# Optimization experiments

Hardware: AMD Instinct MI355X
Metric: run time of the kernel (lower is better)

## Reference

```python
import jax, jax.numpy as jnp
import numpy as np

N = 20000        # nodes
NHID = 128       # hidden channels per head
HEADS = 4
E = 320000       # edges (before self-loops)
NLAYERS = 4
NCLASS = 40
DT, ALPHA, GAMMA = 1.0, 1.0, 1.0
NEG_SLOPE = 0.2  # PyG GATConv default


def setup_inputs() -> dict:
    key = jax.random.key(0)
    ks = jax.random.split(key, 8)
    s = 1.0 / np.sqrt(NHID)
    x = jax.random.normal(ks[0], (N, NHID), jnp.float32)
    src = jax.random.randint(ks[1], (E,), 0, N, dtype=jnp.int32)
    dst = jax.random.randint(ks[2], (E,), 0, N, dtype=jnp.int32)
    W = jax.random.normal(ks[3], (NHID, HEADS * NHID), jnp.float32) * s
    att_src = jax.random.normal(ks[4], (HEADS, NHID), jnp.float32) * s
    att_dst = jax.random.normal(ks[5], (HEADS, NHID), jnp.float32) * s
    bias = jnp.zeros((HEADS * NHID,), jnp.float32)
    Wr = jax.random.normal(ks[6], (NCLASS, NHID), jnp.float32) * s
    br = jnp.zeros((NCLASS,), jnp.float32)
    return {"x": x, "src": src, "dst": dst, "W": W, "att_src": att_src,
            "att_dst": att_dst, "bias": bias, "Wr": Wr, "br": br}


def reference(x, src, dst, W, att_src, att_dst, bias, Wr, br):
    # add self loops (PyG GATConv default)
    loop = jnp.arange(N, dtype=src.dtype)
    s_idx = jnp.concatenate([src, loop])
    d_idx = jnp.concatenate([dst, loop])

    def gat(X):
        # X: [N, NHID] -> out: [N, HEADS*NHID] (head-major, as PyG concat)
        h = (X @ W).reshape(N, HEADS, NHID)                  # [N,H,C]
        a_s = jnp.einsum('nhc,hc->nh', h, att_src)            # [N,H]
        a_d = jnp.einsum('nhc,hc->nh', h, att_dst)            # [N,H]
        e = jax.nn.leaky_relu(a_s[s_idx] + a_d[d_idx], NEG_SLOPE)  # [Etot,H]
        m = jax.ops.segment_max(e, d_idx, num_segments=N)     # scatter-softmax
        ex = jnp.exp(e - m[d_idx])
        den = jax.ops.segment_sum(ex, d_idx, num_segments=N)
        alpha = ex / den[d_idx]                               # [Etot,H]
        msg = h[s_idx] * alpha[..., None]                     # [Etot,H,C]
        out = jax.ops.segment_sum(msg, d_idx, num_segments=N)  # [N,H,C]
        return out.reshape(N, HEADS * NHID) + bias

    def step(carry, _):
        X, Y = carry
        # view(N, -1, nheads).mean(-1) on head-major [N, H*C] layout
        agg = jax.nn.elu(gat(X)).reshape(N, NHID, HEADS).mean(axis=-1)
        Y2 = Y + DT * (agg - ALPHA * Y - GAMMA * X)
        X2 = X + DT * Y2
        return (X2, Y2), (X2, Y2)

    (Xf, Yf), (Xs, Ys) = jax.lax.scan(step, (x, x), None, length=NLAYERS)
    X_all = jnp.concatenate([x[:, None], jnp.moveaxis(Xs, 0, 1)], axis=1)  # [N,L+1,C]
    Y_all = jnp.concatenate([x[:, None], jnp.moveaxis(Ys, 0, 1)], axis=1)
    out = Xf @ Wr.T + br                                     # [N, NCLASS]
    return out, X_all, Y_all
```

## Files before the change

### kernel.cpp

```cpp
#include <hip/hip_runtime.h>

typedef unsigned short u16;
typedef unsigned int u32;

#define N_NODES 20000
#define NE 320000
#define NLAYERS 4
#define NCLASS 40
#define NEG_SLOPE 0.2f
#define LSTRIDE ((NLAYERS + 1) * 128)

typedef __bf16 bf16x8 __attribute__((ext_vector_type(8)));
typedef float f32x4 __attribute__((ext_vector_type(4)));

__device__ inline u16 f2bf(float f) {
    u32 u = __float_as_uint(f);
    return (u16)((u + 0x7fffu + ((u >> 16) & 1u)) >> 16);
}
__device__ inline float bf2f(u16 u) { return __uint_as_float(((u32)u) << 16); }

__global__ void k_init(const float* __restrict__ x, u16* __restrict__ Xbf,
                       float* __restrict__ Xall, float* __restrict__ Yall,
                       int* __restrict__ counts) {
    int t = blockIdx.x * 256 + threadIdx.x;
    if (t >= N_NODES * 128) return;
    if (t < N_NODES) counts[t] = 1;
    float v = x[t];
    Xbf[t] = f2bf(v);
    int n = t >> 7, c = t & 127;
    int ob = n * LSTRIDE + c;
    Xall[ob] = v;
    Yall[ob] = v;
}

__global__ void k_trans(const float* __restrict__ W, u16* __restrict__ Wt) {
    int t = blockIdx.x * 256 + threadIdx.x;
    int k = t >> 9, col = t & 511;
    Wt[col * 128 + k] = f2bf(W[t]);
}

__global__ __launch_bounds__(256) void k_fold(const float* __restrict__ W,
                                              const float* __restrict__ att_s,
                                              const float* __restrict__ att_d,
                                              float* __restrict__ Vs, float* __restrict__ Vd) {
    int wid = (blockIdx.x * 256 + threadIdx.x) >> 6;
    int lane = threadIdx.x & 63;
    int t = wid >> 2, hd = wid & 3;
    float w0 = W[t * 512 + hd * 128 + lane];
    float w1 = W[t * 512 + hd * 128 + 64 + lane];
    float s1 = w0 * att_s[hd * 128 + lane] + w1 * att_s[hd * 128 + 64 + lane];
    float s2 = w0 * att_d[hd * 128 + lane] + w1 * att_d[hd * 128 + 64 + lane];
    for (int off = 32; off; off >>= 1) {
        s1 += __shfl_xor(s1, off);
        s2 += __shfl_xor(s2, off);
    }
    if (lane == 0) {
        Vs[t * 4 + hd] = s1;
        Vd[t * 4 + hd] = s2;
    }
}

__global__ void k_count(const int* __restrict__ dst, int* __restrict__ counts) {
    int t = blockIdx.x * 256 + threadIdx.x;
    if (t < NE) atomicAdd(&counts[dst[t]], 1);
}
__global__ void k_scan(const int* __restrict__ counts, int* __restrict__ indptr,
                       int* __restrict__ cursor) {
    __shared__ int part[1024];
    int t = threadIdx.x;
    const int CH = 20;
    int c0 = t * CH;
    int s = 0;
    for (int i = 0; i < CH; i++) {
        int idx = c0 + i;
        if (idx < N_NODES) s += counts[idx];
    }
    part[t] = s;
    __syncthreads();
    for (int off = 1; off < 1024; off <<= 1) {
        int v = 0;
        if (t >= off) v = part[t - off];
        __syncthreads();
        if (t >= off) part[t] += v;
        __syncthreads();
    }
    int ex = (t == 0) ? 0 : part[t - 1];
    for (int i = 0; i < CH; i++) {
        int idx = c0 + i;
        if (idx < N_NODES) {
            indptr[idx] = ex;
            cursor[idx] = ex;
            ex += counts[idx];
        }
    }
    if (t == 1023) indptr[N_NODES] = part[1023];
}
__global__ void k_scatter(const int* __restrict__ src, const int* __restrict__ dst,
                          int* __restrict__ cursor, int* __restrict__ esrc) {
    int t = blockIdx.x * 256 + threadIdx.x;
    if (t >= NE + N_NODES) return;
    int s, d;
    if (t < NE) { s = src[t]; d = dst[t]; }
    else { s = d = t - NE; }
    int pos = atomicAdd(&cursor[d], 1);
    esrc[pos] = s;
}

__global__ __launch_bounds__(256) void k_att(const float* __restrict__ Xall, int layer,
                                             const float* __restrict__ Vs,
                                             const float* __restrict__ Vd,
                                             float* __restrict__ a_s, float* __restrict__ a_d) {
    int wid = (blockIdx.x * 256 + threadIdx.x) >> 6;
    int lane = threadIdx.x & 63;
    const float* Xr = Xall + wid * LSTRIDE + layer * 128;
    float x0 = Xr[lane], x1 = Xr[64 + lane];
    f32x4 vs0 = *(const f32x4*)(Vs + lane * 4), vs1 = *(const f32x4*)(Vs + (64 + lane) * 4);
    f32x4 vd0 = *(const f32x4*)(Vd + lane * 4), vd1 = *(const f32x4*)(Vd + (64 + lane) * 4);
    f32x4 ps = x0 * vs0 + x1 * vs1;
    f32x4 pd = x0 * vd0 + x1 * vd1;
    for (int off = 32; off; off >>= 1)
        for (int c = 0; c < 4; c++) {
            ps[c] += __shfl_xor(ps[c], off);
            pd[c] += __shfl_xor(pd[c], off);
        }
    if (lane == 0) {
        *(f32x4*)(a_s + wid * 4) = ps;
        *(f32x4*)(a_d + wid * 4) = pd;
    }
}

__global__ __launch_bounds__(256) void k_aggr(
    const int* __restrict__ indptr, const int* __restrict__ esrc,
    const float* __restrict__ a_s, const float* __restrict__ a_d,
    const u16* __restrict__ Xbf, u16* __restrict__ Xagg) {
    __shared__ int s_sh[4][66];
    __shared__ alignas(16) float al_sh[4][66][4];
    int d = (blockIdx.x * 256 + threadIdx.x) >> 6;
    int lane = threadIdx.x & 63;
    int w = threadIdx.x >> 6;
    int start = indptr[d], end = indptr[d + 1];
    int deg = end - start;
    f32x4 ad = *(const f32x4*)(a_d + d * 4);
    f32x4 accA = {0.f, 0.f, 0.f, 0.f};
    f32x4 accB = {0.f, 0.f, 0.f, 0.f};

    auto chunk_aggr = [&](int cnt) {
        int s_cur = s_sh[w][0];
        f32x4 al_cur = *(const f32x4*)&al_sh[w][0][0];
        u32 xv = *(const u32*)(Xbf + s_cur * 128 + lane * 2);
        for (int i = 0; i < cnt; i++) {
            int s_nxt = s_sh[w][i + 1];
            f32x4 al_nxt = *(const f32x4*)&al_sh[w][i + 1][0];
            u32 xv_n = *(const u32*)(Xbf + s_nxt * 128 + lane * 2);
            float x0 = __uint_as_float(xv << 16);
            float x1 = __uint_as_float(xv & 0xffff0000u);
            accA += al_cur * x0;
            accB += al_cur * x1;
            xv = xv_n;
            al_cur = al_nxt;
        }
    };

    if (deg <= 64) {
        int j = start + lane;
        int s = 0;
        f32x4 e = {-1e30f, -1e30f, -1e30f, -1e30f};
        if (j < end) {
            s = esrc[j];
            f32x4 as = *(const f32x4*)(a_s + s * 4);
            for (int c = 0; c < 4; c++) {
                float v = as[c] + ad[c];
                e[c] = v > 0.f ? v : NEG_SLOPE * v;
            }
        }
        f32x4 mx = e;
        for (int off = 32; off; off >>= 1)
            for (int c = 0; c < 4; c++) mx[c] = fmaxf(mx[c], __shfl_xor(mx[c], off));
        f32x4 p;
        for (int c = 0; c < 4; c++) p[c] = __expf(e[c] - mx[c]);
        f32x4 den = p;
        for (int off = 32; off; off >>= 1)
            for (int c = 0; c < 4; c++) den[c] += __shfl_xor(den[c], off);
        f32x4 alpha;
        for (int c = 0; c < 4; c++) alpha[c] = p[c] * (1.f / den[c]);
        s_sh[w][lane] = s;
        *(f32x4*)&al_sh[w][lane][0] = alpha;
        if (lane == 63) {
            s_sh[w][64] = 0;
            f32x4 z = {0.f, 0.f, 0.f, 0.f};
            *(f32x4*)&al_sh[w][64][0] = z;
        }
        __builtin_amdgcn_wave_barrier();
        chunk_aggr(deg);
    } else {
        f32x4 mx = {-1e30f, -1e30f, -1e30f, -1e30f};
        for (int j = start + lane; j < end; j += 64) {
            int s = esrc[j];
            f32x4 e = *(const f32x4*)(a_s + s * 4) + ad;
            for (int c = 0; c < 4; c++) {
                float v = e[c];
                v = v > 0.f ? v : NEG_SLOPE * v;
                mx[c] = fmaxf(mx[c], v);
            }
        }
        for (int off = 32; off; off >>= 1)
            for (int c = 0; c < 4; c++) mx[c] = fmaxf(mx[c], __shfl_xor(mx[c], off));
        f32x4 den = {0.f, 0.f, 0.f, 0.f};
        for (int j = start + lane; j < end; j += 64) {
            int s = esrc[j];
            f32x4 e = *(const f32x4*)(a_s + s * 4) + ad;
            for (int c = 0; c < 4; c++) {
                float v = e[c];
                v = v > 0.f ? v : NEG_SLOPE * v;
                den[c] += __expf(v - mx[c]);
            }
        }
        for (int off = 32; off; off >>= 1)
            for (int c = 0; c < 4; c++) den[c] += __shfl_xor(den[c], off);
        f32x4 rd;
        for (int c = 0; c < 4; c++) rd[c] = 1.f / den[c];
        for (int base = start; base < end; base += 64) {
            int cnt = min(64, end - base);
            int jj = base + lane;
            int s = 0;
            f32x4 alpha = {0.f, 0.f, 0.f, 0.f};
            if (jj < end) {
                s = esrc[jj];
                f32x4 e = *(const f32x4*)(a_s + s * 4) + ad;
                for (int c = 0; c < 4; c++) {
                    float v = e[c];
                    v = v > 0.f ? v : NEG_SLOPE * v;
                    alpha[c] = __expf(v - mx[c]) * rd[c];
                }
            }
            s_sh[w][lane] = s;
            *(f32x4*)&al_sh[w][lane][0] = alpha;
            if (lane == 63) {
                s_sh[w][64] = 0;
                f32x4 z = {0.f, 0.f, 0.f, 0.f};
                *(f32x4*)&al_sh[w][64][0] = z;
            }
            __builtin_amdgcn_wave_barrier();
            chunk_aggr(cnt);
            __builtin_amdgcn_wave_barrier();
        }
    }

    u16* xo = Xagg + d * 512 + lane * 2;
    for (int hh = 0; hh < 4; hh++) {
        u32 pk = (u32)f2bf(accA[hh]) | ((u32)f2bf(accB[hh]) << 16);
        *(u32*)(xo + hh * 128) = pk;
    }
}

__global__ __launch_bounds__(512) void k_fuse(
    const u16* __restrict__ Xagg, const u16* __restrict__ Wt,
    const float* __restrict__ bias,
    float* __restrict__ Xall, float* __restrict__ Yall, u16* __restrict__ Xbf,
    float* __restrict__ a_s_nxt, float* __restrict__ a_d_nxt,
    const float* __restrict__ Vs, const float* __restrict__ Vd,
    int layer, int do_logits) {
    __shared__ u16 As[16 * 520];
    __shared__ float G[16 * 528];
    __shared__ float aggbuf[16 * 130];
    const int t = threadIdx.x;
    const int r0 = blockIdx.x * 16;
    const int wv = t >> 6, lane = t & 63;
    const int h = wv >> 1, colhalf = wv & 1;
    const int lrow = lane & 15, quad = lane >> 4;

    bf16x8 bfr[16];
    {
        const u16* Wb = Wt + (h * 128 + colhalf * 64) * 128;
        for (int k4 = 0; k4 < 4; k4++)
            for (int ni = 0; ni < 4; ni++)
                bfr[k4 * 4 + ni] =
                    *(const bf16x8*)(Wb + (ni * 16 + lrow) * 128 + k4 * 32 + quad * 8);
    }
    for (int i = 0; i < 2; i++) {
        int flat = i * 512 + t;
        int row = flat >> 6, kc = flat & 63;
        *(uint4*)(As + row * 520 + kc * 8) = *(const uint4*)(Xagg + (r0 + row) * 512 + kc * 8);
    }
    __syncthreads();
    f32x4 acc[4] = {};
    for (int k4 = 0; k4 < 4; k4++) {
        bf16x8 a = *(const bf16x8*)(As + lrow * 520 + h * 128 + k4 * 32 + quad * 8);
        for (int ni = 0; ni < 4; ni++)
            acc[ni] = __builtin_amdgcn_mfma_f32_16x16x32_bf16(a, bfr[k4 * 4 + ni], acc[ni], 0, 0, 0);
    }
    for (int ni = 0; ni < 4; ni++) {
        int c = colhalf * 64 + ni * 16 + lrow;
        float bv = bias[h * 128 + c];
        for (int r = 0; r < 4; r++) {
            float v = acc[ni][r] + bv;
            v = v > 0.f ? v : __expf(v) - 1.f;
            G[(quad * 4 + r) * 528 + h * 128 + c] = v;
        }
    }
    __syncthreads();
    {
        int c = t & 127, rg = t >> 7;
        int hh = c >> 5, cc = (c & 31) * 4;
        for (int rr = 0; rr < 4; rr++) {
            int row = rg * 4 + rr;
            f32x4 gp = *(const f32x4*)&G[row * 528 + hh * 128 + cc];
            float agg = 0.25f * (gp[0] + gp[1] + gp[2] + gp[3]);
            aggbuf[row * 130 + c] = agg;
            int node = r0 + row;
            int xo = node * LSTRIDE + layer * 128 + c;
            int no = node * LSTRIDE + (layer + 1) * 128 + c;
            float xp = Xall[xo];
            Xall[no] = agg;
            Yall[no] = agg - xp;
            Xbf[node * 128 + c] = f2bf(agg);
        }
    }
    if (do_logits) {
        __syncthreads();
        f32x4 vs0 = *(const f32x4*)(Vs + lane * 4), vs1 = *(const f32x4*)(Vs + (64 + lane) * 4);
        f32x4 vd0 = *(const f32x4*)(Vd + lane * 4), vd1 = *(const f32x4*)(Vd + (64 + lane) * 4);
        for (int rr = 0; rr < 2; rr++) {
            int row = wv * 2 + rr;
            float x0 = aggbuf[row * 130 + lane], x1 = aggbuf[row * 130 + 64 + lane];
            f32x4 ps = x0 * vs0 + x1 * vs1;
            f32x4 pd = x0 * vd0 + x1 * vd1;
            for (int off = 32; off; off >>= 1)
                for (int c2 = 0; c2 < 4; c2++) {
                    ps[c2] += __shfl_xor(ps[c2], off);
                    pd[c2] += __shfl_xor(pd[c2], off);
                }
            if (lane == 0) {
                int node = r0 + row;
                *(f32x4*)(a_s_nxt + node * 4) = ps;
                *(f32x4*)(a_d_nxt + node * 4) = pd;
            }
        }
    }
}

__global__ __launch_bounds__(256) void k_out(const float* __restrict__ Xall,
                                             const float* __restrict__ Wr,
                                             const float* __restrict__ br,
                                             float* __restrict__ out) {
    __shared__ float Xs[4][128];
    int wave = threadIdx.x >> 6, lane = threadIdx.x & 63;
    int n = blockIdx.x * 4 + wave;
    const float* Xr = Xall + n * LSTRIDE + NLAYERS * 128;
    Xs[wave][lane] = Xr[lane];
    Xs[wave][64 + lane] = Xr[64 + lane];
    __syncthreads();
    if (lane < NCLASS) {
        float acc = 0.f;
        for (int kc = 0; kc < 32; kc++) {
            f32x4 wv = *(const f32x4*)(Wr + lane * 128 + kc * 4);
            for (int q = 0; q < 4; q++) acc += Xs[wave][kc * 4 + q] * wv[q];
        }
        out[n * NCLASS + lane] = acc + br[lane];
    }
}

extern "C" void kernel_launch(void* const* d_in, const int* in_sizes, int n_in,
                              void* d_out, int out_size, void* d_ws, size_t ws_size,
                              hipStream_t stream) {
    const float* x = (const float*)d_in[0];
    const int* src = (const int*)d_in[1];
    const int* dst = (const int*)d_in[2];
    const float* W = (const float*)d_in[3];
    const float* att_s = (const float*)d_in[4];
    const float* att_d = (const float*)d_in[5];
    const float* bias = (const float*)d_in[6];
    const float* Wr = (const float*)d_in[7];
    const float* br = (const float*)d_in[8];

    float* out = (float*)d_out;
    float* Xall = out + (size_t)N_NODES * NCLASS;
    float* Yall = Xall + (size_t)N_NODES * LSTRIDE;

    char* p = (char*)d_ws;
    auto alloc = [&](size_t bytes) -> char* {
        char* r = p;
        p += (bytes + 255) & ~(size_t)255;
        return r;
    };
    u16* Xbf = (u16*)alloc((size_t)N_NODES * 128 * 2);
    u16* Xagg = (u16*)alloc((size_t)N_NODES * 512 * 2);
    u16* Wt = (u16*)alloc(512 * 128 * 2);
    float* a_sA = (float*)alloc((size_t)N_NODES * 4 * 4);
    float* a_dA = (float*)alloc((size_t)N_NODES * 4 * 4);
    float* a_sB = (float*)alloc((size_t)N_NODES * 4 * 4);
    float* a_dB = (float*)alloc((size_t)N_NODES * 4 * 4);
    float* Vs = (float*)alloc(128 * 4 * 4);
    float* Vd = (float*)alloc(128 * 4 * 4);
    int* indptr = (int*)alloc((N_NODES + 1) * 4);
    int* cursor = (int*)alloc(N_NODES * 4);
    int* counts = (int*)alloc(N_NODES * 4);
    int* esrc = (int*)alloc((size_t)(NE + N_NODES) * 4);

    k_init<<<(N_NODES * 128 + 255) / 256, 256, 0, stream>>>(x, Xbf, Xall, Yall, counts);
    k_trans<<<(512 * 128) / 256, 256, 0, stream>>>(W, Wt);
    k_fold<<<128, 256, 0, stream>>>(W, att_s, att_d, Vs, Vd);
    k_count<<<(NE + 255) / 256, 256, 0, stream>>>(dst, counts);
    k_scan<<<1, 1024, 0, stream>>>(counts, indptr, cursor);
    k_scatter<<<(NE + N_NODES + 255) / 256, 256, 0, stream>>>(src, dst, cursor, esrc);

    k_att<<<N_NODES / 4, 256, 0, stream>>>(Xall, 0, Vs, Vd, a_sA, a_dA);

    for (int layer = 0; layer < NLAYERS; layer++) {
        const float* as_r = (layer & 1) ? a_sB : a_sA;
        const float* ad_r = (layer & 1) ? a_dB : a_dA;
        float* as_w = (layer & 1) ? a_sA : a_sB;
        float* ad_w = (layer & 1) ? a_dA : a_dB;
        k_aggr<<<N_NODES / 4, 256, 0, stream>>>(indptr, esrc, as_r, ad_r, Xbf, Xagg);
        k_fuse<<<N_NODES / 16, 512, 0, stream>>>(Xagg, Wt, bias, Xall, Yall, Xbf,
                                                 as_w, ad_w, Vs, Vd, layer,
                                                 (layer + 1 < NLAYERS) ? 1 : 0);
    }
    k_out<<<N_NODES / 4, 256, 0, stream>>>(Xall, Wr, br, out);
}
```

Before: 500.8 us.

## Fuse edge aggregation with MFMA projection per layer and merge setup kernels

Merges the per-layer aggregation and GEMM/ELU/update kernels into one kernel. Each wave aggregates two destination nodes and writes the bf16 aggregate straight to shared memory, so the Xagg global round trip goes away. The bf16 feature buffer is double-buffered so that other blocks never read rows that are already being overwritten. The setup kernels are grouped into two multi-role launches, with a memset and a +1 in the scan standing in for self-loop counts. The head-mean now uses shuffles in place of a large shared G buffer, and W fragments are read from global memory inside the MFMA loop instead of being preloaded into registers.

```diff
diff --git a/kernel.cpp b/kernel.cpp
--- a/kernel.cpp
+++ b/kernel.cpp
@@ -17,84 +17,110 @@
     u32 u = __float_as_uint(f);
     return (u16)((u + 0x7fffu + ((u >> 16) & 1u)) >> 16);
 }
-__device__ inline float bf2f(u16 u) { return __uint_as_float(((u32)u) << 16); }
-
-__global__ void k_init(const float* __restrict__ x, u16* __restrict__ Xbf,
-                       float* __restrict__ Xall, float* __restrict__ Yall,
-                       int* __restrict__ counts) {
-    int t = blockIdx.x * 256 + threadIdx.x;
-    if (t >= N_NODES * 128) return;
-    if (t < N_NODES) counts[t] = 1;
-    float v = x[t];
-    Xbf[t] = f2bf(v);
-    int n = t >> 7, c = t & 127;
-    int ob = n * LSTRIDE + c;
-    Xall[ob] = v;
-    Yall[ob] = v;
-}
-
-__global__ void k_trans(const float* __restrict__ W, u16* __restrict__ Wt) {
-    int t = blockIdx.x * 256 + threadIdx.x;
-    int k = t >> 9, col = t & 511;
-    Wt[col * 128 + k] = f2bf(W[t]);
-}
-
-__global__ __launch_bounds__(256) void k_fold(const float* __restrict__ W,
-                                              const float* __restrict__ att_s,
-                                              const float* __restrict__ att_d,
-                                              float* __restrict__ Vs, float* __restrict__ Vd) {
-    int wid = (blockIdx.x * 256 + threadIdx.x) >> 6;
-    int lane = threadIdx.x & 63;
-    int t = wid >> 2, hd = wid & 3;
-    float w0 = W[t * 512 + hd * 128 + lane];
-    float w1 = W[t * 512 + hd * 128 + 64 + lane];
-    float s1 = w0 * att_s[hd * 128 + lane] + w1 * att_s[hd * 128 + 64 + lane];
-    float s2 = w0 * att_d[hd * 128 + lane] + w1 * att_d[hd * 128 + 64 + lane];
-    for (int off = 32; off; off >>= 1) {
-        s1 += __shfl_xor(s1, off);
-        s2 += __shfl_xor(s2, off);
-    }
-    if (lane == 0) {
-        Vs[t * 4 + hd] = s1;
-        Vd[t * 4 + hd] = s2;
-    }
-}
-
-__global__ void k_count(const int* __restrict__ dst, int* __restrict__ counts) {
-    int t = blockIdx.x * 256 + threadIdx.x;
-    if (t < NE) atomicAdd(&counts[dst[t]], 1);
-}
-__global__ void k_scan(const int* __restrict__ counts, int* __restrict__ indptr,
-                       int* __restrict__ cursor) {
-    __shared__ int part[1024];
-    int t = threadIdx.x;
-    const int CH = 20;
-    int c0 = t * CH;
-    int s = 0;
-    for (int i = 0; i < CH; i++) {
-        int idx = c0 + i;
-        if (idx < N_NODES) s += counts[idx];
-    }
-    part[t] = s;
-    __syncthreads();
-    for (int off = 1; off < 1024; off <<= 1) {
-        int v = 0;
-        if (t >= off) v = part[t - off];
+__device__ inline u32 pack2bf(float lo, float hi) {
+    return (u32)f2bf(lo) | ((u32)f2bf(hi) << 16);
+}
+
+#define P1_INIT 10000
+#define P1_TRANS 256
+#define P1_FOLD 128
+#define P1_COUNT 1250
+__global__ __launch_bounds__(256) void k_pre1(
+    const float* __restrict__ x, const int* __restrict__ dst,
+    const float* __restrict__ W, const float* __restrict__ att_s,
+    const float* __restrict__ att_d,
+    u16* __restrict__ Xbf, float* __restrict__ Xall, float* __restrict__ Yall,
+    u16* __restrict__ Wt, float* __restrict__ Vs, float* __restrict__ Vd,
+    int* __restrict__ counts) {
+    int b = blockIdx.x;
+    if (b < P1_INIT) {
+        int t = b * 256 + threadIdx.x;
+        float v = x[t];
+        Xbf[t] = f2bf(v);
+        int n = t >> 7, c = t & 127;
+        int ob = n * LSTRIDE + c;
+        Xall[ob] = v;
+        Yall[ob] = v;
+    } else if (b < P1_INIT + P1_TRANS) {
+        int t = (b - P1_INIT) * 256 + threadIdx.x;
+        int k = t >> 9, col = t & 511;
+        Wt[col * 128 + k] = f2bf(W[t]);
+    } else if (b < P1_INIT + P1_TRANS + P1_FOLD) {
+        int wid = ((b - P1_INIT - P1_TRANS) * 256 + threadIdx.x) >> 6;
+        int lane = threadIdx.x & 63;
+        int t = wid >> 2, hd = wid & 3;
+        float w0 = W[t * 512 + hd * 128 + lane];
+        float w1 = W[t * 512 + hd * 128 + 64 + lane];
+        float s1 = w0 * att_s[hd * 128 + lane] + w1 * att_s[hd * 128 + 64 + lane];
+        float s2 = w0 * att_d[hd * 128 + lane] + w1 * att_d[hd * 128 + 64 + lane];
+        for (int off = 32; off; off >>= 1) {
+            s1 += __shfl_xor(s1, off);
+            s2 += __shfl_xor(s2, off);
+        }
+        if (lane == 0) {
+            Vs[t * 4 + hd] = s1;
+            Vd[t * 4 + hd] = s2;
+        }
+    } else {
+        int t = (b - P1_INIT - P1_TRANS - P1_FOLD) * 256 + threadIdx.x;
+        atomicAdd(&counts[dst[t]], 1);
+    }
+}
+
+__global__ __launch_bounds__(1024) void k_pre2(
+    const int* __restrict__ counts, int* __restrict__ indptr, int* __restrict__ cursor,
+    const float* __restrict__ x, const float* __restrict__ Vs, const float* __restrict__ Vd,
+    float* __restrict__ a_s, float* __restrict__ a_d) {
+    if (blockIdx.x == 0) {
+        __shared__ int part[1024];
+        int t = threadIdx.x;
+        const int CH = 20;
+        int c0 = t * CH;
+        int s = 0;
+        for (int i = 0; i < CH; i++) {
+            int idx = c0 + i;
+            if (idx < N_NODES) s += counts[idx] + 1;
+        }
+        part[t] = s;
         __syncthreads();
-        if (t >= off) part[t] += v;
-        __syncthreads();
-    }
-    int ex = (t == 0) ? 0 : part[t - 1];
-    for (int i = 0; i < CH; i++) {
-        int idx = c0 + i;
-        if (idx < N_NODES) {
-            indptr[idx] = ex;
-            cursor[idx] = ex;
-            ex += counts[idx];
-        }
-    }
-    if (t == 1023) indptr[N_NODES] = part[1023];
-}
+        for (int off = 1; off < 1024; off <<= 1) {
+            int v = 0;
+            if (t >= off) v = part[t - off];
+            __syncthreads();
+            if (t >= off) part[t] += v;
+            __syncthreads();
+        }
+        int ex = (t == 0) ? 0 : part[t - 1];
+        for (int i = 0; i < CH; i++) {
+            int idx = c0 + i;
+            if (idx < N_NODES) {
+                indptr[idx] = ex;
+                cursor[idx] = ex;
+                ex += counts[idx] + 1;
+            }
+        }
+        if (t == 1023) indptr[N_NODES] = part[1023];
+    } else {
+        int wave = threadIdx.x >> 6, lane = threadIdx.x & 63;
+        int n = (blockIdx.x - 1) * 16 + wave;
+        const float* Xr = x + n * 128;
+        float x0 = Xr[lane], x1 = Xr[64 + lane];
+        f32x4 vs0 = *(const f32x4*)(Vs + lane * 4), vs1 = *(const f32x4*)(Vs + (64 + lane) * 4);
+        f32x4 vd0 = *(const f32x4*)(Vd + lane * 4), vd1 = *(const f32x4*)(Vd + (64 + lane) * 4);
+        f32x4 ps = x0 * vs0 + x1 * vs1;
+        f32x4 pd = x0 * vd0 + x1 * vd1;
+        for (int off = 32; off; off >>= 1)
+            for (int c = 0; c < 4; c++) {
+                ps[c] += __shfl_xor(ps[c], off);
+                pd[c] += __shfl_xor(pd[c], off);
+            }
+        if (lane == 0) {
+            *(f32x4*)(a_s + n * 4) = ps;
+            *(f32x4*)(a_d + n * 4) = pd;
+        }
+    }
+}
+
 __global__ void k_scatter(const int* __restrict__ src, const int* __restrict__ dst,
                           int* __restrict__ cursor, int* __restrict__ esrc) {
     int t = blockIdx.x * 256 + threadIdx.x;
@@ -106,66 +132,37 @@
     esrc[pos] = s;
 }
 
-__global__ __launch_bounds__(256) void k_att(const float* __restrict__ Xall, int layer,
-                                             const float* __restrict__ Vs,
-                                             const float* __restrict__ Vd,
-                                             float* __restrict__ a_s, float* __restrict__ a_d) {
-    int wid = (blockIdx.x * 256 + threadIdx.x) >> 6;
-    int lane = threadIdx.x & 63;
-    const float* Xr = Xall + wid * LSTRIDE + layer * 128;
-    float x0 = Xr[lane], x1 = Xr[64 + lane];
-    f32x4 vs0 = *(const f32x4*)(Vs + lane * 4), vs1 = *(const f32x4*)(Vs + (64 + lane) * 4);
-    f32x4 vd0 = *(const f32x4*)(Vd + lane * 4), vd1 = *(const f32x4*)(Vd + (64 + lane) * 4);
-    f32x4 ps = x0 * vs0 + x1 * vs1;
-    f32x4 pd = x0 * vd0 + x1 * vd1;
-    for (int off = 32; off; off >>= 1)
-        for (int c = 0; c < 4; c++) {
-            ps[c] += __shfl_xor(ps[c], off);
-            pd[c] += __shfl_xor(pd[c], off);
-        }
-    if (lane == 0) {
-        *(f32x4*)(a_s + wid * 4) = ps;
-        *(f32x4*)(a_d + wid * 4) = pd;
-    }
-}
-
-__global__ __launch_bounds__(256) void k_aggr(
+__global__ __launch_bounds__(512) void k_layer(
     const int* __restrict__ indptr, const int* __restrict__ esrc,
     const float* __restrict__ a_s, const float* __restrict__ a_d,
-    const u16* __restrict__ Xbf, u16* __restrict__ Xagg) {
-    __shared__ int s_sh[4][66];
-    __shared__ alignas(16) float al_sh[4][66][4];
-    int d = (blockIdx.x * 256 + threadIdx.x) >> 6;
-    int lane = threadIdx.x & 63;
-    int w = threadIdx.x >> 6;
-    int start = indptr[d], end = indptr[d + 1];
-    int deg = end - start;
-    f32x4 ad = *(const f32x4*)(a_d + d * 4);
-    f32x4 accA = {0.f, 0.f, 0.f, 0.f};
-    f32x4 accB = {0.f, 0.f, 0.f, 0.f};
-
-    auto chunk_aggr = [&](int cnt) {
-        int s_cur = s_sh[w][0];
-        f32x4 al_cur = *(const f32x4*)&al_sh[w][0][0];
-        u32 xv = *(const u32*)(Xbf + s_cur * 128 + lane * 2);
-        for (int i = 0; i < cnt; i++) {
-            int s_nxt = s_sh[w][i + 1];
-            f32x4 al_nxt = *(const f32x4*)&al_sh[w][i + 1][0];
-            u32 xv_n = *(const u32*)(Xbf + s_nxt * 128 + lane * 2);
-            float x0 = __uint_as_float(xv << 16);
-            float x1 = __uint_as_float(xv & 0xffff0000u);
-            accA += al_cur * x0;
-            accB += al_cur * x1;
-            xv = xv_n;
-            al_cur = al_nxt;
-        }
-    };
-
-    if (deg <= 64) {
-        int j = start + lane;
+    const u16* __restrict__ XbfR, const u16* __restrict__ Wt,
+    const float* __restrict__ bias,
+    float* __restrict__ Xall, float* __restrict__ Yall, u16* __restrict__ XbfW,
+    float* __restrict__ a_s_nxt, float* __restrict__ a_d_nxt,
+    const float* __restrict__ Vs, const float* __restrict__ Vd,
+    int layer, int do_logits) {
+    __shared__ int s_sh[8][2][66];
+    __shared__ alignas(16) float al_sh[8][2][66][4];
+    __shared__ u16 As[16 * 520];
+    __shared__ float aggbuf[16 * 130];
+    const int t = threadIdx.x;
+    const int r0 = blockIdx.x * 16;
+    const int w = t >> 6, lane = t & 63;
+
+    f32x4 acc00 = {0.f, 0.f, 0.f, 0.f}, acc01 = {0.f, 0.f, 0.f, 0.f};
+    f32x4 acc10 = {0.f, 0.f, 0.f, 0.f}, acc11 = {0.f, 0.f, 0.f, 0.f};
+    int d0 = r0 + w * 2;
+    int st0 = indptr[d0], en0 = indptr[d0 + 1], en1 = indptr[d0 + 2];
+    int st1 = en0;
+    int deg0 = en0 - st0, deg1 = en1 - st1;
+    f32x4 ad0 = *(const f32x4*)(a_d + d0 * 4);
+    f32x4 ad1 = *(const f32x4*)(a_d + d0 * 4 + 4);
+
+    auto prep = [&](int nd, int st, int en, f32x4 ad) {
+        int j = st + lane;
         int s = 0;
         f32x4 e = {-1e30f, -1e30f, -1e30f, -1e30f};
-        if (j < end) {
+        if (j < en) {
             s = esrc[j];
             f32x4 as = *(const f32x4*)(a_s + s * 4);
             for (int c = 0; c < 4; c++) {
@@ -183,18 +180,31 @@
             for (int c = 0; c < 4; c++) den[c] += __shfl_xor(den[c], off);
         f32x4 alpha;
         for (int c = 0; c < 4; c++) alpha[c] = p[c] * (1.f / den[c]);
-        s_sh[w][lane] = s;
-        *(f32x4*)&al_sh[w][lane][0] = alpha;
+        s_sh[w][nd][lane] = s;
+        *(f32x4*)al_sh[w][nd][lane] = alpha;
         if (lane == 63) {
-            s_sh[w][64] = 0;
+            s_sh[w][nd][64] = 0;
             f32x4 z = {0.f, 0.f, 0.f, 0.f};
-            *(f32x4*)&al_sh[w][64][0] = z;
-        }
-        __builtin_amdgcn_wave_barrier();
-        chunk_aggr(deg);
-    } else {
+            *(f32x4*)al_sh[w][nd][64] = z;
+        }
+    };
+    auto chunk1 = [&](int nd, int cnt, f32x4& aL, f32x4& aH) {
+        int sc = s_sh[w][nd][0];
+        f32x4 al = *(const f32x4*)al_sh[w][nd][0];
+        u32 xv = *(const u32*)(XbfR + sc * 128 + lane * 2);
+        for (int i = 0; i < cnt; i++) {
+            int sn = s_sh[w][nd][i + 1];
+            f32x4 an = *(const f32x4*)al_sh[w][nd][i + 1];
+            u32 xn = *(const u32*)(XbfR + sn * 128 + lane * 2);
+            aL += al * __uint_as_float(xv << 16);
+            aH += al * __uint_as_float(xv & 0xffff0000u);
+            xv = xn;
+            al = an;
+        }
+    };
+    auto gen = [&](int nd, int st, int en, f32x4 ad, f32x4& aL, f32x4& aH) {
         f32x4 mx = {-1e30f, -1e30f, -1e30f, -1e30f};
-        for (int j = start + lane; j < end; j += 64) {
+        for (int j = st + lane; j < en; j += 64) {
             int s = esrc[j];
             f32x4 e = *(const f32x4*)(a_s + s * 4) + ad;
             for (int c = 0; c < 4; c++) {
@@ -206,7 +216,7 @@
         for (int off = 32; off; off >>= 1)
             for (int c = 0; c < 4; c++) mx[c] = fmaxf(mx[c], __shfl_xor(mx[c], off));
         f32x4 den = {0.f, 0.f, 0.f, 0.f};
-        for (int j = start + lane; j < end; j += 64) {
+        for (int j = st + lane; j < en; j += 64) {
             int s = esrc[j];
             f32x4 e = *(const f32x4*)(a_s + s * 4) + ad;
             for (int c = 0; c < 4; c++) {
@@ -219,12 +229,12 @@
             for (int c = 0; c < 4; c++) den[c] += __shfl_xor(den[c], off);
         f32x4 rd;
         for (int c = 0; c < 4; c++) rd[c] = 1.f / den[c];
-        for (int base = start; base < end; base += 64) {
-            int cnt = min(64, end - base);
+        for (int base = st; base < en; base += 64) {
+            int cnt = min(64, en - base);
             int jj = base + lane;
             int s = 0;
             f32x4 alpha = {0.f, 0.f, 0.f, 0.f};
-            if (jj < end) {
+            if (jj < en) {
                 s = esrc[jj];
                 f32x4 e = *(const f32x4*)(a_s + s * 4) + ad;
                 for (int c = 0; c < 4; c++) {
@@ -233,95 +243,101 @@
                     alpha[c] = __expf(v - mx[c]) * rd[c];
                 }
             }
-            s_sh[w][lane] = s;
-            *(f32x4*)&al_sh[w][lane][0] = alpha;
+            s_sh[w][nd][lane] = s;
+            *(f32x4*)al_sh[w][nd][lane] = alpha;
             if (lane == 63) {
-                s_sh[w][64] = 0;
+                s_sh[w][nd][64] = 0;
                 f32x4 z = {0.f, 0.f, 0.f, 0.f};
-                *(f32x4*)&al_sh[w][64][0] = z;
+                *(f32x4*)al_sh[w][nd][64] = z;
             }
             __builtin_amdgcn_wave_barrier();
-            chunk_aggr(cnt);
+            chunk1(nd, cnt, aL, aH);
             __builtin_amdgcn_wave_barrier();
         }
-    }
-
-    u16* xo = Xagg + d * 512 + lane * 2;
-    for (int hh = 0; hh < 4; hh++) {
-        u32 pk = (u32)f2bf(accA[hh]) | ((u32)f2bf(accB[hh]) << 16);
-        *(u32*)(xo + hh * 128) = pk;
-    }
-}
-
-__global__ __launch_bounds__(512) void k_fuse(
-    const u16* __restrict__ Xagg, const u16* __restrict__ Wt,
-    const float* __restrict__ bias,
-    float* __restrict__ Xall, float* __restrict__ Yall, u16* __restrict__ Xbf,
-    float* __restrict__ a_s_nxt, float* __restrict__ a_d_nxt,
-    const float* __restrict__ Vs, const float* __restrict__ Vd,
-    int layer, int do_logits) {
-    __shared__ u16 As[16 * 520];
-    __shared__ float G[16 * 528];
-    __shared__ float aggbuf[16 * 130];
-    const int t = threadIdx.x;
-    const int r0 = blockIdx.x * 16;
-    const int wv = t >> 6, lane = t & 63;
-    const int h = wv >> 1, colhalf = wv & 1;
+    };
+
+    if (deg0 <= 64 && deg1 <= 64) {
+        prep(0, st0, en0, ad0);
+        prep(1, st1, en1, ad1);
+        __builtin_amdgcn_wave_barrier();
+        int cm = deg0 > deg1 ? deg0 : deg1;
+        int sA = s_sh[w][0][0], sB = s_sh[w][1][0];
+        f32x4 aA = *(const f32x4*)al_sh[w][0][0];
+        f32x4 aB = *(const f32x4*)al_sh[w][1][0];
+        u32 xA = *(const u32*)(XbfR + sA * 128 + lane * 2);
+        u32 xB = *(const u32*)(XbfR + sB * 128 + lane * 2);
+        for (int i = 0; i < cm; i++) {
+            int sA2 = s_sh[w][0][i + 1], sB2 = s_sh[w][1][i + 1];
+            f32x4 aA2 = *(const f32x4*)al_sh[w][0][i + 1];
+            f32x4 aB2 = *(const f32x4*)al_sh[w][1][i + 1];
+            u32 xA2 = *(const u32*)(XbfR + sA2 * 128 + lane * 2);
+            u32 xB2 = *(const u32*)(XbfR + sB2 * 128 + lane * 2);
+            acc00 += aA * __uint_as_float(xA << 16);
+            acc01 += aA * __uint_as_float(xA & 0xffff0000u);
+            acc10 += aB * __uint_as_float(xB << 16);
+            acc11 += aB * __uint_as_float(xB & 0xffff0000u);
+            xA = xA2; aA = aA2; xB = xB2; aB = aB2;
+        }
+    } else {
+        gen(0, st0, en0, ad0, acc00, acc01);
+        gen(1, st1, en1, ad1, acc10, acc11);
+    }
+
+    {
+        u16* a0 = As + (w * 2) * 520 + lane * 2;
+        u16* a1 = As + (w * 2 + 1) * 520 + lane * 2;
+        for (int h = 0; h < 4; h++) {
+            *(u32*)(a0 + h * 128) = pack2bf(acc00[h], acc01[h]);
+            *(u32*)(a1 + h * 128) = pack2bf(acc10[h], acc11[h]);
+        }
+    }
+    __syncthreads();
+
+    const int h = w >> 1, colhalf = w & 1;
     const int lrow = lane & 15, quad = lane >> 4;
-
-    bf16x8 bfr[16];
-    {
-        const u16* Wb = Wt + (h * 128 + colhalf * 64) * 128;
-        for (int k4 = 0; k4 < 4; k4++)
-            for (int ni = 0; ni < 4; ni++)
-                bfr[k4 * 4 + ni] =
-                    *(const bf16x8*)(Wb + (ni * 16 + lrow) * 128 + k4 * 32 + quad * 8);
-    }
-    for (int i = 0; i < 2; i++) {
-        int flat = i * 512 + t;
-        int row = flat >> 6, kc = flat & 63;
-        *(uint4*)(As + row * 520 + kc * 8) = *(const uint4*)(Xagg + (r0 + row) * 512 + kc * 8);
-    }
-    __syncthreads();
-    f32x4 acc[4] = {};
+    f32x4 macc[4] = {};
     for (int k4 = 0; k4 < 4; k4++) {
         bf16x8 a = *(const bf16x8*)(As + lrow * 520 + h * 128 + k4 * 32 + quad * 8);
-        for (int ni = 0; ni < 4; ni++)
-            acc[ni] = __builtin_amdgcn_mfma_f32_16x16x32_bf16(a, bfr[k4 * 4 + ni], acc[ni], 0, 0, 0);
+        for (int ni = 0; ni < 4; ni++) {
+            bf16x8 bfrag = *(const bf16x8*)(Wt + (h * 128 + colhalf * 64 + ni * 16 + lrow) * 128 +
+                                            k4 * 32 + quad * 8);
+            macc[ni] = __builtin_amdgcn_mfma_f32_16x16x32_bf16(a, bfrag, macc[ni], 0, 0, 0);
+        }
     }
     for (int ni = 0; ni < 4; ni++) {
-        int c = colhalf * 64 + ni * 16 + lrow;
-        float bv = bias[h * 128 + c];
+        float bv = bias[h * 128 + colhalf * 64 + ni * 16 + lrow];
         for (int r = 0; r < 4; r++) {
-            float v = acc[ni][r] + bv;
+            float v = macc[ni][r] + bv;
             v = v > 0.f ? v : __expf(v) - 1.f;
-            G[(quad * 4 + r) * 528 + h * 128 + c] = v;
+            v += __shfl_xor(v, 1);
+            v += __shfl_xor(v, 2);
+            if ((lrow & 3) == 0) {
+                int row = quad * 4 + r;
+                int cO = h * 32 + colhalf * 16 + ni * 4 + (lrow >> 2);
+                aggbuf[row * 130 + cO] = 0.25f * v;
+            }
         }
     }
     __syncthreads();
+
     {
         int c = t & 127, rg = t >> 7;
-        int hh = c >> 5, cc = (c & 31) * 4;
         for (int rr = 0; rr < 4; rr++) {
             int row = rg * 4 + rr;
-            f32x4 gp = *(const f32x4*)&G[row * 528 + hh * 128 + cc];
-            float agg = 0.25f * (gp[0] + gp[1] + gp[2] + gp[3]);
-            aggbuf[row * 130 + c] = agg;
+            float agg = aggbuf[row * 130 + c];
             int node = r0 + row;
             int xo = node * LSTRIDE + layer * 128 + c;
-            int no = node * LSTRIDE + (layer + 1) * 128 + c;
             float xp = Xall[xo];
-            Xall[no] = agg;
-            Yall[no] = agg - xp;
-            Xbf[node * 128 + c] = f2bf(agg);
+            Xall[xo + 128] = agg;
+            Yall[xo + 128] = agg - xp;
+            XbfW[node * 128 + c] = f2bf(agg);
         }
     }
     if (do_logits) {
-        __syncthreads();
         f32x4 vs0 = *(const f32x4*)(Vs + lane * 4), vs1 = *(const f32x4*)(Vs + (64 + lane) * 4);
         f32x4 vd0 = *(const f32x4*)(Vd + lane * 4), vd1 = *(const f32x4*)(Vd + (64 + lane) * 4);
         for (int rr = 0; rr < 2; rr++) {
-            int row = wv * 2 + rr;
+            int row = w * 2 + rr;
             float x0 = aggbuf[row * 130 + lane], x1 = aggbuf[row * 130 + 64 + lane];
             f32x4 ps = x0 * vs0 + x1 * vs1;
             f32x4 pd = x0 * vd0 + x1 * vd1;
@@ -383,8 +399,8 @@
         p += (bytes + 255) & ~(size_t)255;
         return r;
     };
-    u16* Xbf = (u16*)alloc((size_t)N_NODES * 128 * 2);
-    u16* Xagg = (u16*)alloc((size_t)N_NODES * 512 * 2);
+    u16* XbfA = (u16*)alloc((size_t)N_NODES * 128 * 2);
+    u16* XbfB = (u16*)alloc((size_t)N_NODES * 128 * 2);
     u16* Wt = (u16*)alloc(512 * 128 * 2);
     float* a_sA = (float*)alloc((size_t)N_NODES * 4 * 4);
     float* a_dA = (float*)alloc((size_t)N_NODES * 4 * 4);
@@ -397,24 +413,22 @@
     int* counts = (int*)alloc(N_NODES * 4);
     int* esrc = (int*)alloc((size_t)(NE + N_NODES) * 4);
 
-    k_init<<<(N_NODES * 128 + 255) / 256, 256, 0, stream>>>(x, Xbf, Xall, Yall, counts);
-    k_trans<<<(512 * 128) / 256, 256, 0, stream>>>(W, Wt);
-    k_fold<<<128, 256, 0, stream>>>(W, att_s, att_d, Vs, Vd);
-    k_count<<<(NE + 255) / 256, 256, 0, stream>>>(dst, counts);
-    k_scan<<<1, 1024, 0, stream>>>(counts, indptr, cursor);
+    hipMemsetAsync(counts, 0, N_NODES * sizeof(int), stream);
+    k_pre1<<<P1_INIT + P1_TRANS + P1_FOLD + P1_COUNT, 256, 0, stream>>>(
+        x, dst, W, att_s, att_d, XbfA, Xall, Yall, Wt, Vs, Vd, counts);
+    k_pre2<<<1251, 1024, 0, stream>>>(counts, indptr, cursor, x, Vs, Vd, a_sA, a_dA);
     k_scatter<<<(NE + N_NODES + 255) / 256, 256, 0, stream>>>(src, dst, cursor, esrc);
-
-    k_att<<<N_NODES / 4, 256, 0, stream>>>(Xall, 0, Vs, Vd, a_sA, a_dA);
 
     for (int layer = 0; layer < NLAYERS; layer++) {
         const float* as_r = (layer & 1) ? a_sB : a_sA;
         const float* ad_r = (layer & 1) ? a_dB : a_dA;
         float* as_w = (layer & 1) ? a_sA : a_sB;
         float* ad_w = (layer & 1) ? a_dA : a_dB;
-        k_aggr<<<N_NODES / 4, 256, 0, stream>>>(indptr, esrc, as_r, ad_r, Xbf, Xagg);
-        k_fuse<<<N_NODES / 16, 512, 0, stream>>>(Xagg, Wt, bias, Xall, Yall, Xbf,
-                                                 as_w, ad_w, Vs, Vd, layer,
-                                                 (layer + 1 < NLAYERS) ? 1 : 0);
+        const u16* xr = (layer & 1) ? XbfB : XbfA;
+        u16* xw = (layer & 1) ? XbfA : XbfB;
+        k_layer<<<N_NODES / 16, 512, 0, stream>>>(indptr, esrc, as_r, ad_r, xr, Wt, bias,
+                                                  Xall, Yall, xw, as_w, ad_w, Vs, Vd, layer,
+                                                  (layer + 1 < NLAYERS) ? 1 : 0);
     }
     k_out<<<N_NODES / 4, 256, 0, stream>>>(Xall, Wr, br, out);
 }
```

Measured after the change: 478.1 us. 4.5% less time.
